# Optimization experiments

Measured on AMD Instinct MI355X. Metric: run time of the kernel, lower is better.

Reference implementation:

```python
import jax, jax.numpy as jnp
import numpy as np
from jax import lax

B, C, H, W = 16, 256, 64, 64
K = 3  # kernel_size


def setup_inputs() -> dict:
    key = jax.random.key(0)
    k1, k2, k3, k4 = jax.random.split(key, 4)
    x = jax.random.normal(k1, (B, C, H, W), dtype=jnp.float32)
    # nn.Parameter init is ones; perturb so softmax is non-trivial
    dir_weight_h = jnp.ones((1, C, 1, 1), jnp.float32) + 0.1 * jax.random.normal(k2, (1, C, 1, 1), jnp.float32)
    dir_weight_w = jnp.ones((1, C, 1, 1), jnp.float32) + 0.1 * jax.random.normal(k3, (1, C, 1, 1), jnp.float32)
    gate_w = 0.1 * jax.random.normal(k4, (), jnp.float32)  # 1x1 conv on 1 channel = scalar
    gate_b = jnp.float32(-1.0)  # init.constant_(gate.bias, -1.0)
    return {"x": x, "dir_weight_h": dir_weight_h, "dir_weight_w": dir_weight_w,
            "gate_w": gate_w, "gate_b": gate_b}


def reference(x, dir_weight_h, dir_weight_w, gate_w, gate_b):
    b, c, h, w = x.shape
    # directional softmax-weighted global pooling
    ww = jax.nn.softmax(dir_weight_w, axis=1)            # (1,C,1,1)
    global_h = jnp.mean(x * ww, axis=3, keepdims=True)   # (B,C,H,1)
    wh = jax.nn.softmax(dir_weight_h, axis=1)
    global_w = jnp.mean(x * wh, axis=2, keepdims=True)   # (B,C,1,W)
    global_dir = global_h + global_w                     # broadcast -> (B,C,H,W)

    # local covariance: unfold(x1)*unfold(x2) mean over k*k taps
    # == KxK box-sum of (x1*x2) with zero padding, divided by k*k
    half = c // 2
    prod = x[:, :half] * x[:, half:]                     # (B,C/2,H,W)
    cov = lax.reduce_window(prod, 0.0, lax.add,
                            window_dimensions=(1, 1, K, K),
                            window_strides=(1, 1, 1, 1),
                            padding=[(0, 0), (0, 0), (K // 2, K // 2), (K // 2, K // 2)]) / (K * K)

    consistency = jnp.mean(jnp.abs(cov), axis=1, keepdims=True)  # (B,1,H,W)
    local_anomaly = 1.0 - jnp.clip(consistency, 0.0, 1.0)

    fusion = jnp.mean(global_dir, axis=1, keepdims=True) * local_anomaly  # (B,1,H,W)
    attention = jax.nn.sigmoid(gate_w * fusion + gate_b)  # 1x1 conv with scalar weight/bias
    return x * attention
```

## Files before the change

### kernel.cpp

```cpp
#include <hip/hip_runtime.h>
#include <math.h>

#define NB 16
#define NC 256
#define NH 64
#define NW 64
#define HALF 128
#define PLANE (NH*NW)

#define NT 4
#define UNITS 36
#define TILEF (UNITS*256)

#define WS_ATT 0

#define SCR_GHP 524288
#define SCR_GWP (SCR_GHP + 8192)

typedef __attribute__((address_space(1))) void gvoid;
typedef __attribute__((address_space(3))) void lvoid;

__device__ __forceinline__ void async_load16(const float* g, float* l) {
    __builtin_amdgcn_global_load_lds((gvoid*)(size_t)(const void*)g, (lvoid*)l, 16, 0, 0);
}

__device__ __forceinline__ float sum4(float4 v) { return (v.x+v.y)+(v.z+v.w); }

__global__ __launch_bounds__(256) void k_reduce(const float* __restrict__ x,
                                                const float* __restrict__ dwh,
                                                const float* __restrict__ dww,
                                                float* __restrict__ scr) {
    __shared__ float stage[2*TILEF];
    __shared__ float ew[256], eh[256];
    __shared__ float wsum[8];
    __shared__ float4 ldsc[4][16];

    const int t    = threadIdx.x;
    const int rg   = t >> 6;
    const int lane = t & 63;
    const int pl   = lane & 3;
    const int fc   = lane >> 2;

    const int blk    = blockIdx.x;
    const int pgc    = blk & 7;
    const int stripe = (blk >> 3) & 3;
    const int b      = blk >> 5;
    const int r0s    = stripe * 16;
    const int r0     = r0s + rg*4;

    {
        const float vw = dww[t], vh = dwh[t];
        const float evw = expf(vw), evh = expf(vh);
        ew[t] = evw; eh[t] = evh;
        float sw = evw, sh = evh;
        #pragma unroll
        for (int m = 1; m < 64; m <<= 1) { sw += __shfl_xor(sw, m); sh += __shfl_xor(sh, m); }
        if (lane == 0) { wsum[rg] = sw; wsum[4+rg] = sh; }
    }
    asm volatile("s_waitcnt vmcnt(0) lgkmcnt(0)" ::: "memory");

    const size_t bbase = (size_t)b * NC * PLANE;
    {
        const int pg = pgc*NT;
        #pragma unroll
        for (int i = 0; i < 9; ++i) {
            const int u = rg*9 + i;
            int gr = r0s + (u >> 1) - 1; gr = gr < 0 ? 0 : (gr > 63 ? 63 : gr);
            const int ch = pg*4 + pl + (u & 1)*HALF;
            async_load16(x + bbase + (size_t)ch*PLANE + gr*NW + fc*4, &stage[u*256]);
        }
    }

    const float km0 = (r0 == 0)  ? 0.f : 1.f;
    const float km5 = (r0 == 60) ? 0.f : 1.f;
    float invSw = 0.f, invSh = 0.f;
    float4 c4[4] = {{0,0,0,0},{0,0,0,0},{0,0,0,0},{0,0,0,0}};
    float  ghrow[4] = {0.f,0.f,0.f,0.f};
    float4 colacc = {0.f,0.f,0.f,0.f};

    for (int k = 0; k < NT; ++k) {
        asm volatile("s_waitcnt lgkmcnt(0)" ::: "memory");
        __builtin_amdgcn_s_barrier();

        if (k == 0) {
            invSw = 1.f / ((wsum[0]+wsum[1]) + (wsum[2]+wsum[3]));
            invSh = 1.f / ((wsum[4]+wsum[5]) + (wsum[6]+wsum[7]));
        }
        if (k < NT-1) {
            const int pg = pgc*NT + k + 1;
            float* dstb = &stage[((k+1)&1)*TILEF];
            #pragma unroll
            for (int i = 0; i < 9; ++i) {
                const int u = rg*9 + i;
                int gr = r0s + (u >> 1) - 1; gr = gr < 0 ? 0 : (gr > 63 ? 63 : gr);
                const int ch = pg*4 + pl + (u & 1)*HALF;
                async_load16(x + bbase + (size_t)ch*PLANE + gr*NW + fc*4, dstb + u*256);
            }
            asm volatile("s_waitcnt vmcnt(9)" ::: "memory");
        } else {
            asm volatile("s_waitcnt vmcnt(0)" ::: "memory");
        }
        __builtin_amdgcn_s_barrier();

        const int pg = pgc*NT + k;
        const float ww1 = ew[pg*4+pl]      * invSw;
        const float ww2 = ew[pg*4+pl+HALF] * invSw;
        const float wh1 = eh[pg*4+pl]      * invSh;
        const float wh2 = eh[pg*4+pl+HALF] * invSh;

        const float4* st4 = reinterpret_cast<const float4*>(&stage[(k&1)*TILEF]);
        float4 a[6], bv[6];
        #pragma unroll
        for (int j = 0; j < 6; ++j) {
            const int lr = rg*4 + j;
            a[j]  = st4[(lr*2+0)*64 + lane];
            bv[j] = st4[(lr*2+1)*64 + lane];
        }

        #pragma unroll
        for (int j = 1; j <= 4; ++j) {
            ghrow[j-1] += ww1*sum4(a[j]) + ww2*sum4(bv[j]);
            colacc.x += wh1*a[j].x + wh2*bv[j].x;
            colacc.y += wh1*a[j].y + wh2*bv[j].y;
            colacc.z += wh1*a[j].z + wh2*bv[j].z;
            colacc.w += wh1*a[j].w + wh2*bv[j].w;
        }

        float4 p[6];
        #pragma unroll
        for (int j = 0; j < 6; ++j) {
            p[j].x = a[j].x*bv[j].x; p[j].y = a[j].y*bv[j].y;
            p[j].z = a[j].z*bv[j].z; p[j].w = a[j].w*bv[j].w;
        }
        p[0].x *= km0; p[0].y *= km0; p[0].z *= km0; p[0].w *= km0;
        p[5].x *= km5; p[5].y *= km5; p[5].z *= km5; p[5].w *= km5;

        #pragma unroll
        for (int i = 0; i < 4; ++i) {
            float4 v;
            v.x = p[i].x + p[i+1].x + p[i+2].x;
            v.y = p[i].y + p[i+1].y + p[i+2].y;
            v.z = p[i].z + p[i+1].z + p[i+2].z;
            v.w = p[i].w + p[i+1].w + p[i+2].w;
            float L = __shfl_up(v.w, 4);
            float R = __shfl_down(v.x, 4);
            if (fc == 0)  L = 0.f;
            if (fc == 15) R = 0.f;
            c4[i].x += fabsf(L   + v.x + v.y);
            c4[i].y += fabsf(v.x + v.y + v.z);
            c4[i].z += fabsf(v.y + v.z + v.w);
            c4[i].w += fabsf(v.z + v.w + R);
        }
    }

    const float SC  = 1.0f/(9.0f*128.0f);
    const float GSC = 1.0f/16384.0f;

    #pragma unroll
    for (int i = 0; i < 4; ++i) {
        c4[i].x += __shfl_xor(c4[i].x, 1); c4[i].x += __shfl_xor(c4[i].x, 2);
        c4[i].y += __shfl_xor(c4[i].y, 1); c4[i].y += __shfl_xor(c4[i].y, 2);
        c4[i].z += __shfl_xor(c4[i].z, 1); c4[i].z += __shfl_xor(c4[i].z, 2);
        c4[i].w += __shfl_xor(c4[i].w, 1); c4[i].w += __shfl_xor(c4[i].w, 2);
    }
    if (pl == 0) {
        float4* dst = reinterpret_cast<float4*>(scr) + (pgc << 14) + (b << 10);
        #pragma unroll
        for (int i = 0; i < 4; ++i) {
            float4 s = { c4[i].x*SC, c4[i].y*SC, c4[i].z*SC, c4[i].w*SC };
            dst[(r0 + i)*16 + fc] = s;
        }
    }

    #pragma unroll
    for (int i = 0; i < 4; ++i) {
        float s = ghrow[i];
        s += __shfl_xor(s, 1);  s += __shfl_xor(s, 2);
        s += __shfl_xor(s, 4);  s += __shfl_xor(s, 8);
        s += __shfl_xor(s, 16); s += __shfl_xor(s, 32);
        if (lane == 0) scr[SCR_GHP + (b*NH + r0 + i)*8 + pgc] = s * GSC;
    }

    colacc.x += __shfl_xor(colacc.x, 1); colacc.x += __shfl_xor(colacc.x, 2);
    colacc.y += __shfl_xor(colacc.y, 1); colacc.y += __shfl_xor(colacc.y, 2);
    colacc.z += __shfl_xor(colacc.z, 1); colacc.z += __shfl_xor(colacc.z, 2);
    colacc.w += __shfl_xor(colacc.w, 1); colacc.w += __shfl_xor(colacc.w, 2);
    if (pl == 0) ldsc[rg][fc] = colacc;
    __syncthreads();
    if (t < 16) {
        float4 s0 = ldsc[0][t], s1 = ldsc[1][t], s2 = ldsc[2][t], s3 = ldsc[3][t];
        float4 s;
        s.x = ((s0.x+s1.x)+(s2.x+s3.x)) * GSC;
        s.y = ((s0.y+s1.y)+(s2.y+s3.y)) * GSC;
        s.z = ((s0.z+s1.z)+(s2.z+s3.z)) * GSC;
        s.w = ((s0.w+s1.w)+(s2.w+s3.w)) * GSC;
        *reinterpret_cast<float4*>(scr + SCR_GWP + (size_t)(pgc*4 + stripe)*1024 + b*NW + t*4) = s;
    }
}

__global__ __launch_bounds__(256) void k_att(float* __restrict__ ws,
                                             const float* __restrict__ scr,
                                             const float* __restrict__ pgw,
                                             const float* __restrict__ pgb) {
    __shared__ __align__(16) float sgh[64];
    __shared__ __align__(16) float sgw[64];
    const int t = threadIdx.x;
    const int b = blockIdx.x >> 2;
    const int q = blockIdx.x & 3;

    if (t < 64) {
        float acc = 0.f;
        #pragma unroll 4
        for (int j = 0; j < 32; ++j) acc += scr[SCR_GWP + (size_t)j*1024 + b*NW + t];
        sgw[t] = acc;
    } else if (t < 128) {
        const int r = t - 64;
        float acc = 0.f;
        const float* g = scr + SCR_GHP + (b*NH + r)*8;
        #pragma unroll
        for (int s2 = 0; s2 < 8; ++s2) acc += g[s2];
        sgh[r] = acc;
    }
    __syncthreads();

    const int u = (b << 10) + (q << 8) + t;
    const float4* cp = reinterpret_cast<const float4*>(scr);
    float4 s = {0.f,0.f,0.f,0.f};
    #pragma unroll
    for (int g = 0; g < 8; ++g) {
        const float4 v = cp[(g << 14) + u];
        s.x += v.x; s.y += v.y; s.z += v.z; s.w += v.w;
    }
    const int h  = (u >> 4) & 63;
    const int w4 = u & 15;
    const float ghv  = sgh[h];
    const float4 gwv = *reinterpret_cast<const float4*>(&sgw[w4*4]);
    const float gW = pgw[0], gB = pgb[0];

    float4 o;
    float z;
    z = gW*(ghv+gwv.x)*(1.f - fminf(fmaxf(s.x,0.f),1.f)) + gB; o.x = 1.f/(1.f+expf(-z));
    z = gW*(ghv+gwv.y)*(1.f - fminf(fmaxf(s.y,0.f),1.f)) + gB; o.y = 1.f/(1.f+expf(-z));
    z = gW*(ghv+gwv.z)*(1.f - fminf(fmaxf(s.z,0.f),1.f)) + gB; o.z = 1.f/(1.f+expf(-z));
    z = gW*(ghv+gwv.w)*(1.f - fminf(fmaxf(s.w,0.f),1.f)) + gB; o.w = 1.f/(1.f+expf(-z));
    reinterpret_cast<float4*>(ws + WS_ATT)[u] = o;
}

__global__ __launch_bounds__(256) void k_apply(const float* __restrict__ x,
                                               const float* __restrict__ ws,
                                               float* __restrict__ out) {
    const float* att = ws + WS_ATT;
    const int total4 = NB*NC*NH*NW/4;
    const int stride = gridDim.x * blockDim.x;
    for (int i = blockIdx.x*blockDim.x + threadIdx.x; i < total4; i += stride) {
        const int w4 = i & 15;
        const int h  = (i >> 4) & 63;
        const int b  = i >> 18;
        const float4 xv = reinterpret_cast<const float4*>(x)[i];
        const float4 av = reinterpret_cast<const float4*>(att)[(b << 10) + (h << 4) + w4];
        float4 o;
        o.x = xv.x*av.x; o.y = xv.y*av.y; o.z = xv.z*av.z; o.w = xv.w*av.w;
        reinterpret_cast<float4*>(out)[i] = o;
    }
}

extern "C" void kernel_launch(void* const* d_in, const int* in_sizes, int n_in,
                              void* d_out, int out_size, void* d_ws, size_t ws_size,
                              hipStream_t stream) {
    const float* x   = (const float*)d_in[0];
    const float* dwh = (const float*)d_in[1];
    const float* dww = (const float*)d_in[2];
    const float* pgw = (const float*)d_in[3];
    const float* pgb = (const float*)d_in[4];
    float* out = (float*)d_out;
    float* ws  = (float*)d_ws;
    float* scr = out;

    k_reduce<<<NB*4*8, 256, 0, stream>>>(x, dwh, dww, scr);
    k_att<<<64, 256, 0, stream>>>(ws, scr, pgw, pgb);
    k_apply<<<2048, 256, 0, stream>>>(x, ws, out);
}
```

Baseline: 47.31 us.

## Restage tiles as contiguous row units with register halos and padded LDS

The staging of each channel tile into LDS changes from per-row 256-float units that included duplicated halo rows to 16-row contiguous units with 260-float padding. Each wave now loads one full 256-byte row per async load, and the halo rows for the edge waves are fetched with direct global loads into registers. This trims the async loads per thread from 9 to 8, drops the redundant halo rows, and the padding aims to avoid LDS bank conflicts. The column-partial scratch layout is also transposed so the attention kernel can reduce each row with contiguous float4 loads, at the cost of extra register pressure and more complex waitcnt accounting.

```diff
diff --git a/kernel.cpp b/kernel.cpp
--- a/kernel.cpp
+++ b/kernel.cpp
@@ -9,8 +9,8 @@
 #define PLANE (NH*NW)
 
 #define NT 4
-#define UNITS 36
-#define TILEF (UNITS*256)
+#define S_UNIT 260
+#define TILEF (32*S_UNIT)
 
 #define WS_ATT 0
 
@@ -48,6 +48,9 @@
     const int r0s    = stripe * 16;
     const int r0     = r0s + rg*4;
 
+    const bool edge = (rg == 0) || (rg == 3);
+    const size_t bbase = (size_t)b * NC * PLANE;
+
     {
         const float vw = dww[t], vh = dwh[t];
         const float evw = expf(vw), evh = expf(vh);
@@ -59,17 +62,28 @@
     }
     asm volatile("s_waitcnt vmcnt(0) lgkmcnt(0)" ::: "memory");
 
-    const size_t bbase = (size_t)b * NC * PLANE;
-    {
-        const int pg = pgc*NT;
-        #pragma unroll
-        for (int i = 0; i < 9; ++i) {
-            const int u = rg*9 + i;
-            int gr = r0s + (u >> 1) - 1; gr = gr < 0 ? 0 : (gr > 63 ? 63 : gr);
-            const int ch = pg*4 + pl + (u & 1)*HALF;
-            async_load16(x + bbase + (size_t)ch*PLANE + gr*NW + fc*4, &stage[u*256]);
-        }
-    }
+    auto issue_tile = [&](int tk) {
+        const int pg = pgc*NT + tk;
+        float* dstb = &stage[(tk & 1) * TILEF];
+        #pragma unroll
+        for (int i = 0; i < 8; ++i) {
+            const int u   = rg*8 + i;
+            const int chh = u >> 2;
+            const int rq  = u & 3;
+            const int cg  = pg*4 + (chh & 3) + (chh >> 2)*HALF;
+            const float* src = x + bbase + (size_t)cg*PLANE + (size_t)(r0s + rq*4)*NW + lane*4;
+            async_load16(src, dstb + u*S_UNIT);
+        }
+    };
+    auto load_halo = [&](int tk, float4& ha, float4& hb) {
+        if (edge) {
+            int hr = (rg == 0) ? r0s - 1 : r0s + 16;
+            hr = hr < 0 ? 0 : (hr > 63 ? 63 : hr);
+            const int c1 = (pgc*NT + tk)*4 + pl;
+            ha = *reinterpret_cast<const float4*>(x + bbase + (size_t)c1*PLANE + hr*NW + fc*4);
+            hb = *reinterpret_cast<const float4*>(x + bbase + (size_t)(c1+HALF)*PLANE + hr*NW + fc*4);
+        }
+    };
 
     const float km0 = (r0 == 0)  ? 0.f : 1.f;
     const float km5 = (r0 == 60) ? 0.f : 1.f;
@@ -78,43 +92,50 @@
     float  ghrow[4] = {0.f,0.f,0.f,0.f};
     float4 colacc = {0.f,0.f,0.f,0.f};
 
-    for (int k = 0; k < NT; ++k) {
+    float4 haA = {0,0,0,0}, hbA = {0,0,0,0};
+    float4 haB = {0,0,0,0}, hbB = {0,0,0,0};
+
+    issue_tile(0);
+    load_halo(0, haA, hbA);
+
+    auto tile_iter = [&](int tk, const float4& haU, const float4& hbU,
+                         float4& haL, float4& hbL) {
         asm volatile("s_waitcnt lgkmcnt(0)" ::: "memory");
         __builtin_amdgcn_s_barrier();
 
-        if (k == 0) {
+        if (tk == 0) {
             invSw = 1.f / ((wsum[0]+wsum[1]) + (wsum[2]+wsum[3]));
             invSh = 1.f / ((wsum[4]+wsum[5]) + (wsum[6]+wsum[7]));
         }
-        if (k < NT-1) {
-            const int pg = pgc*NT + k + 1;
-            float* dstb = &stage[((k+1)&1)*TILEF];
-            #pragma unroll
-            for (int i = 0; i < 9; ++i) {
-                const int u = rg*9 + i;
-                int gr = r0s + (u >> 1) - 1; gr = gr < 0 ? 0 : (gr > 63 ? 63 : gr);
-                const int ch = pg*4 + pl + (u & 1)*HALF;
-                async_load16(x + bbase + (size_t)ch*PLANE + gr*NW + fc*4, dstb + u*256);
-            }
-            asm volatile("s_waitcnt vmcnt(9)" ::: "memory");
+        if (tk < NT-1) {
+            issue_tile(tk + 1);
+            load_halo(tk + 1, haL, hbL);
+            if (edge) asm volatile("s_waitcnt vmcnt(10)" ::: "memory");
+            else      asm volatile("s_waitcnt vmcnt(8)"  ::: "memory");
         } else {
             asm volatile("s_waitcnt vmcnt(0)" ::: "memory");
         }
         __builtin_amdgcn_s_barrier();
 
-        const int pg = pgc*NT + k;
+        const int pg = pgc*NT + tk;
         const float ww1 = ew[pg*4+pl]      * invSw;
         const float ww2 = ew[pg*4+pl+HALF] * invSw;
         const float wh1 = eh[pg*4+pl]      * invSh;
         const float wh2 = eh[pg*4+pl+HALF] * invSh;
 
-        const float4* st4 = reinterpret_cast<const float4*>(&stage[(k&1)*TILEF]);
+        const float* buf = &stage[(tk & 1) * TILEF];
         float4 a[6], bv[6];
         #pragma unroll
         for (int j = 0; j < 6; ++j) {
-            const int lr = rg*4 + j;
-            a[j]  = st4[(lr*2+0)*64 + lane];
-            bv[j] = st4[(lr*2+1)*64 + lane];
+            const int lr = rg*4 - 1 + j;
+            if (j == 0 && rg == 0) { a[j] = haU; bv[j] = hbU; }
+            else if (j == 5 && rg == 3) { a[j] = haU; bv[j] = hbU; }
+            else {
+                const int uA  = pl*4 + (lr >> 2);
+                const int off = (lr & 3)*64 + fc*4;
+                a[j]  = *reinterpret_cast<const float4*>(buf + uA*S_UNIT + off);
+                bv[j] = *reinterpret_cast<const float4*>(buf + (uA+16)*S_UNIT + off);
+            }
         }
 
         #pragma unroll
@@ -151,7 +172,12 @@
             c4[i].z += fabsf(v.y + v.z + v.w);
             c4[i].w += fabsf(v.z + v.w + R);
         }
-    }
+    };
+
+    tile_iter(0, haA, hbA, haB, hbB);
+    tile_iter(1, haB, hbB, haA, hbA);
+    tile_iter(2, haA, hbA, haB, hbB);
+    tile_iter(3, haB, hbB, haA, hbA);
 
     const float SC  = 1.0f/(9.0f*128.0f);
     const float GSC = 1.0f/16384.0f;
@@ -187,14 +213,10 @@
     colacc.w += __shfl_xor(colacc.w, 1); colacc.w += __shfl_xor(colacc.w, 2);
     if (pl == 0) ldsc[rg][fc] = colacc;
     __syncthreads();
-    if (t < 16) {
-        float4 s0 = ldsc[0][t], s1 = ldsc[1][t], s2 = ldsc[2][t], s3 = ldsc[3][t];
-        float4 s;
-        s.x = ((s0.x+s1.x)+(s2.x+s3.x)) * GSC;
-        s.y = ((s0.y+s1.y)+(s2.y+s3.y)) * GSC;
-        s.z = ((s0.z+s1.z)+(s2.z+s3.z)) * GSC;
-        s.w = ((s0.w+s1.w)+(s2.w+s3.w)) * GSC;
-        *reinterpret_cast<float4*>(scr + SCR_GWP + (size_t)(pgc*4 + stripe)*1024 + b*NW + t*4) = s;
+    if (t < 64) {
+        const float* lf = reinterpret_cast<const float*>(ldsc);
+        float s = (lf[t] + lf[64+t]) + (lf[128+t] + lf[192+t]);
+        scr[SCR_GWP + (b*NW + t)*32 + pgc*4 + stripe] = s * GSC;
     }
 }
 
@@ -209,17 +231,14 @@
     const int q = blockIdx.x & 3;
 
     if (t < 64) {
-        float acc = 0.f;
-        #pragma unroll 4
-        for (int j = 0; j < 32; ++j) acc += scr[SCR_GWP + (size_t)j*1024 + b*NW + t];
+        const float4* gp = reinterpret_cast<const float4*>(scr + SCR_GWP + (b*NW + t)*32);
+        float acc = ((sum4(gp[0])+sum4(gp[1])) + (sum4(gp[2])+sum4(gp[3])))
+                  + ((sum4(gp[4])+sum4(gp[5])) + (sum4(gp[6])+sum4(gp[7])));
         sgw[t] = acc;
     } else if (t < 128) {
         const int r = t - 64;
-        float acc = 0.f;
-        const float* g = scr + SCR_GHP + (b*NH + r)*8;
-        #pragma unroll
-        for (int s2 = 0; s2 < 8; ++s2) acc += g[s2];
-        sgh[r] = acc;
+        const float4* gp = reinterpret_cast<const float4*>(scr + SCR_GHP + (b*NH + r)*8);
+        sgh[r] = sum4(gp[0]) + sum4(gp[1]);
     }
     __syncthreads();
 
```

After: 48.53 us. 1.03x slower.
